# Performance work log

Measured on AMD Instinct MI355X. Metric: run time of the kernel, lower is better.

The kernel has to match this reference:

```python
import jax, jax.numpy as jnp
import numpy as np

EPS = 1e-8

def setup_inputs() -> dict:
    key = jax.random.key(0)
    k1, k2, k3 = jax.random.split(key, 3)
    b, c, h, w = 64, 20, 128, 128
    x = jax.random.normal(k1, (b, c, h, w), dtype=jnp.float32)
    y = jax.random.randint(k2, (b, c), 0, 2).astype(jnp.int32)
    threshold_p = jnp.zeros((b, c, h * w), dtype=jnp.float32)
    fg = jax.random.uniform(k3, (b, c), dtype=jnp.float32)
    return {"x": x, "y": y, "threshold_p": threshold_p, "fg": fg, "iter": 0}

def reference(x, y, threshold_p, fg, iter):
    b, c, h, w = x.shape
    hw = h * w
    xs = jax.nn.sigmoid(x.reshape(b, c, hw))  # [b,c,hw]
    yf = y.astype(xs.dtype)
    if iter % 100 < 80:
        # per-row descending sort, pick the fg*(h*w)-th value as threshold
        srt = -jnp.sort(-xs.reshape(b * c, hw), axis=1)  # descending
        idx = (fg.reshape(-1) * hw).astype(jnp.int32)  # [b*c]
        thr = jnp.take_along_axis(srt, idx[:, None], axis=1).reshape(b, c, 1)
        thr = jax.lax.stop_gradient(thr)
    else:
        thr = jax.nn.sigmoid(jnp.mean(threshold_p.reshape(b, c, hw), axis=2))[:, :, None]
        xs = jax.lax.stop_gradient(xs)
    thr = jnp.clip(thr, 0.0001)  # [b,c,1], broadcasts over hw
    y_ = yf[:, :, None]  # [b,c,1] broadcast equivalent of stacking hw copies
    mask_low = jax.lax.stop_gradient((xs <= thr).astype(xs.dtype) * y_)
    mask_high = jax.lax.stop_gradient((xs > thr).astype(xs.dtype) * y_)
    h_low = (-(xs * xs) / (thr * thr) + 2.0 * xs / thr) * mask_low
    alpha = 1.0 / jnp.clip((1.0 - thr) ** 2, EPS)
    h_high = alpha * (1.0 - xs) * (1.0 - 2.0 * thr + xs) * mask_high
    if iter % 100 < 80:
        neg_loss = -(1.0 - y_) * jnp.log(jnp.clip(1.0 - xs, EPS))
        loss = jnp.mean(h_high + h_low + neg_loss)
    else:
        loss = jnp.sum(h_low) / jnp.sum(mask_low) + jnp.sum(h_high) / jnp.sum(mask_high)
    return loss
```

## Files before the change

### kernel.cpp

```cpp
#include <hip/hip_runtime.h>

#define HW     16384
#define NROWS  1280
#define NT     512
#define NWAVES (NT / 64)
#define CAP    1024
#define NBIN1  4096

__device__ __forceinline__ unsigned f2u(float f) {
    unsigned u = __float_as_uint(f);
    unsigned m = (unsigned)((int)u >> 31);
    return u ^ (m | 0x80000000u);
}
__device__ __forceinline__ float u2f(unsigned u) {
    u = (u & 0x80000000u) ? (u & 0x7fffffffu) : ~u;
    return __uint_as_float(u);
}

__device__ __forceinline__ void wave_scan_pick(
    const unsigned* h, int bins_per_lane, int stride, unsigned kk,
    unsigned* s_bin, unsigned* s_k)
{
    const int lane = threadIdx.x & 63;
    const int base = lane * bins_per_lane;
    unsigned local = 0;
    for (int j = 0; j < bins_per_lane; ++j) {
        int b = base + j;
        local += h[stride * b] + (stride == 2 ? h[stride * b + 1] : 0u);
    }
    unsigned s = local;
    #pragma unroll
    for (int off = 1; off < 64; off <<= 1) {
        unsigned t = __shfl_down(s, off, 64);
        if (lane + off < 64) s += t;
    }
    const unsigned above = s - local;
    if (s > kk && above <= kk) {
        unsigned run = above;
        for (int j = bins_per_lane - 1; j >= 0; --j) {
            int b = base + j;
            unsigned c = h[stride * b] + (stride == 2 ? h[stride * b + 1] : 0u);
            if (run + c > kk) { *s_bin = (unsigned)b; *s_k = kk - run; break; }
            run += c;
        }
    }
}

__global__ __launch_bounds__(NT) void spatial_bce_row(
    const float* __restrict__ x, const int* __restrict__ y,
    const float* __restrict__ fg, double* __restrict__ partial)
{
    __shared__ unsigned hist[NBIN1 * 2];
    __shared__ unsigned buf[CAP];
    __shared__ unsigned s_cnt, s_bin, s_k;
    __shared__ float    swf[NWAVES][4];
    __shared__ int      swi[NWAVES];
    __shared__ double   swd[NWAVES];

    const int row  = blockIdx.x;
    const int tid  = threadIdx.x;
    const int lane = tid & 63;
    const int wid  = tid >> 6;
    const float4* x4 = (const float4*)(x + (size_t)row * HW);
    const float L2E   = 1.44269504f;
    const float LN2   = 0.69314718f;
    const float NLCAP = 18.420680744f;

    const int yrow = y[row];

    if (yrow == 0) {
        float a0 = 0.f, a1 = 0.f, a2 = 0.f, a3 = 0.f;
        for (int i = tid; i < HW / 4; i += NT) {
            float4 v = x4[i];
            a0 += fminf(v.x + LN2 * log2f(1.f + exp2f(-L2E * v.x)), NLCAP);
            a1 += fminf(v.y + LN2 * log2f(1.f + exp2f(-L2E * v.y)), NLCAP);
            a2 += fminf(v.z + LN2 * log2f(1.f + exp2f(-L2E * v.z)), NLCAP);
            a3 += fminf(v.w + LN2 * log2f(1.f + exp2f(-L2E * v.w)), NLCAP);
        }
        double acc = (double)((a0 + a1) + (a2 + a3));
        #pragma unroll
        for (int off = 32; off > 0; off >>= 1) acc += __shfl_down(acc, off, 64);
        if (lane == 0) swd[wid] = acc;
        __syncthreads();
        if (tid == 0) {
            double t = 0.0;
            for (int w = 0; w < NWAVES; ++w) t += swd[w];
            partial[row] = t;
        }
        return;
    }

    {
        uint4 z = {0u, 0u, 0u, 0u};
        for (int i = tid; i < NBIN1 * 2 / 4; i += NT) ((uint4*)hist)[i] = z;
    }
    if (tid == 0) {
        int k = (int)(fg[row] * (float)HW);
        k = max(0, min(HW - 1, k));
        s_k = (unsigned)k; s_cnt = 0u;
    }
    __syncthreads();
    const unsigned k0 = s_k;

    const int rep = tid & 1;
    for (int i = tid; i < HW / 4; i += NT) {
        float4 v = x4[i];
        atomicAdd(&hist[2 * (f2u(v.x) >> 20) + rep], 1u);
        atomicAdd(&hist[2 * (f2u(v.y) >> 20) + rep], 1u);
        atomicAdd(&hist[2 * (f2u(v.z) >> 20) + rep], 1u);
        atomicAdd(&hist[2 * (f2u(v.w) >> 20) + rep], 1u);
    }
    __syncthreads();
    if (tid < 64) wave_scan_pick(hist, NBIN1 / 64, 2, k0, &s_bin, &s_k);
    __syncthreads();
    const unsigned bin1 = s_bin;
    const unsigned k1   = s_k;

    float sL = 0.f, s2L = 0.f, sH = 0.f, s2H = 0.f;
    int   nH = 0;
    for (int i = tid; i < HW / 4; i += NT) {
        float4 v = x4[i];
        float e[4] = {v.x, v.y, v.z, v.w};
        #pragma unroll
        for (int j = 0; j < 4; ++j) {
            float xv = e[j];
            unsigned u = f2u(xv);
            unsigned b = u >> 20;
            float t  = exp2f(-L2E * xv);
            float s  = __builtin_amdgcn_rcpf(1.0f + t);
            float s2 = s * s;
            if (b < bin1)      { sL += s; s2L += s2; }
            else if (b > bin1) { sH += s; s2H += s2; ++nH; }
            else { unsigned p = atomicAdd(&s_cnt, 1u); if (p < CAP) buf[p] = u; }
        }
    }
    __syncthreads();
    const unsigned cnt = s_cnt;

    unsigned ustar;
    if (cnt <= CAP) {
        for (int i = tid; i < 1024; i += NT) hist[i] = 0u;
        __syncthreads();
        for (int c = tid; c < (int)cnt; c += NT)
            atomicAdd(&hist[(buf[c] >> 10) & 1023u], 1u);
        __syncthreads();
        if (tid < 64) wave_scan_pick(hist, 16, 1, k1, &s_bin, &s_k);
        __syncthreads();
        const unsigned pfx22 = (bin1 << 10) | s_bin;
        const unsigned k2    = s_k;
        for (int i = tid; i < 1024; i += NT) hist[i] = 0u;
        __syncthreads();
        for (int c = tid; c < (int)cnt; c += NT)
            if ((buf[c] >> 10) == pfx22) atomicAdd(&hist[buf[c] & 1023u], 1u);
        __syncthreads();
        if (tid < 64) wave_scan_pick(hist, 16, 1, k2, &s_bin, &s_k);
        __syncthreads();
        ustar = (pfx22 << 10) | s_bin;
    } else {
        for (int i = tid; i < 1024; i += NT) hist[i] = 0u;
        __syncthreads();
        for (int i = tid; i < HW / 4; i += NT) {
            float4 v = x4[i];
            unsigned u[4] = {f2u(v.x), f2u(v.y), f2u(v.z), f2u(v.w)};
            #pragma unroll
            for (int j = 0; j < 4; ++j)
                if ((u[j] >> 20) == bin1) atomicAdd(&hist[(u[j] >> 10) & 1023u], 1u);
        }
        __syncthreads();
        if (tid < 64) wave_scan_pick(hist, 16, 1, k1, &s_bin, &s_k);
        __syncthreads();
        const unsigned pfx22 = (bin1 << 10) | s_bin;
        const unsigned k2    = s_k;
        for (int i = tid; i < 1024; i += NT) hist[i] = 0u;
        __syncthreads();
        for (int i = tid; i < HW / 4; i += NT) {
            float4 v = x4[i];
            unsigned u[4] = {f2u(v.x), f2u(v.y), f2u(v.z), f2u(v.w)};
            #pragma unroll
            for (int j = 0; j < 4; ++j)
                if ((u[j] >> 10) == pfx22) atomicAdd(&hist[u[j] & 1023u], 1u);
        }
        __syncthreads();
        if (tid < 64) wave_scan_pick(hist, 16, 1, k2, &s_bin, &s_k);
        __syncthreads();
        ustar = (pfx22 << 10) | s_bin;
    }

    const float xk = u2f(ustar);
    float thr = 1.0f / (1.0f + expf(-xk));
    thr = fmaxf(thr, 1e-4f);

    if (cnt <= CAP) {
        for (int c = tid; c < (int)cnt; c += NT) {
            float xv = u2f(buf[c]);
            float t  = exp2f(-L2E * xv);
            float s  = __builtin_amdgcn_rcpf(1.0f + t);
            float s2 = s * s;
            if (s > thr) { sH += s; s2H += s2; ++nH; }
            else         { sL += s; s2L += s2; }
        }
    } else {
        for (int i = tid; i < HW / 4; i += NT) {
            float4 v = x4[i];
            float e[4] = {v.x, v.y, v.z, v.w};
            #pragma unroll
            for (int j = 0; j < 4; ++j) {
                unsigned u = f2u(e[j]);
                if ((u >> 20) == bin1) {
                    float t  = exp2f(-L2E * e[j]);
                    float s  = __builtin_amdgcn_rcpf(1.0f + t);
                    float s2 = s * s;
                    if (s > thr) { sH += s; s2H += s2; ++nH; }
                    else         { sL += s; s2L += s2; }
                }
            }
        }
    }

    #pragma unroll
    for (int off = 32; off > 0; off >>= 1) {
        sL  += __shfl_down(sL,  off, 64);
        s2L += __shfl_down(s2L, off, 64);
        sH  += __shfl_down(sH,  off, 64);
        s2H += __shfl_down(s2H, off, 64);
        nH  += __shfl_down(nH,  off, 64);
    }
    if (lane == 0) {
        swf[wid][0] = sL; swf[wid][1] = s2L; swf[wid][2] = sH; swf[wid][3] = s2H;
        swi[wid] = nH;
    }
    __syncthreads();
    if (tid == 0) {
        double SL = 0, S2L = 0, SH = 0, S2H = 0; double NH = 0;
        for (int w = 0; w < NWAVES; ++w) {
            SL += swf[w][0]; S2L += swf[w][1]; SH += swf[w][2]; S2H += swf[w][3];
            NH += (double)swi[w];
        }
        const double t   = (double)thr;
        const double omt = 1.0 - t;
        const double a   = 1.0 / fmax(omt * omt, 1e-8);
        const double low  = 2.0 * SL / t - S2L / (t * t);
        const double high = a * (NH * (1.0 - 2.0 * t) - S2H + 2.0 * t * SH);
        partial[row] = low + high;
    }
}

__global__ __launch_bounds__(256) void spatial_bce_final(
    const double* __restrict__ partial, float* __restrict__ out)
{
    __shared__ double sred[256];
    double acc = 0.0;
    for (int i = threadIdx.x; i < NROWS; i += 256) acc += partial[i];
    sred[threadIdx.x] = acc;
    __syncthreads();
    for (int off = 128; off > 0; off >>= 1) {
        if (threadIdx.x < off) sred[threadIdx.x] += sred[threadIdx.x + off];
        __syncthreads();
    }
    if (threadIdx.x == 0)
        out[0] = (float)(sred[0] / ((double)NROWS * (double)HW));
}

extern "C" void kernel_launch(void* const* d_in, const int* in_sizes, int n_in,
                              void* d_out, int out_size, void* d_ws, size_t ws_size,
                              hipStream_t stream) {
    const float* x  = (const float*)d_in[0];
    const int*   y  = (const int*)d_in[1];
    const float* fg = (const float*)d_in[3];

    double* partial = (double*)d_ws;

    spatial_bce_row<<<NROWS, NT, 0, stream>>>(x, y, fg, partial);
    spatial_bce_final<<<1, 256, 0, stream>>>(partial, (float*)d_out);
}
```

Measured before the change: 44.35 us.

## Keep row in registers and replace candidate buffer with on-the-fly sub-histograms

Each thread loads its 32 row elements into registers once and reuses them for every radix-select pass, instead of re-reading global memory each pass. The shared candidate buffer and its overflow fallback are removed. The second-level histogram is built during the moments pass and the third level from the registers, and classification compares bit keys rather than sigmoids. Shared histograms are padded to spread bank conflicts, and the softplus for negative rows is rewritten in a numerically stable form. In exchange, register pressure rises, which may lower occupancy.

```diff
diff --git a/kernel.cpp b/kernel.cpp
--- a/kernel.cpp
+++ b/kernel.cpp
@@ -4,8 +4,11 @@
 #define NROWS  1280
 #define NT     512
 #define NWAVES (NT / 64)
-#define CAP    1024
+#define NCHUNK (HW / 4 / NT)
 #define NBIN1  4096
+#define SEG1   (NBIN1 + NBIN1/32)
+#define NSUB   1024
+#define SEGS   (NSUB + NSUB/32)
 
 __device__ __forceinline__ unsigned f2u(float f) {
     unsigned u = __float_as_uint(f);
@@ -16,17 +19,20 @@
     u = (u & 0x80000000u) ? (u & 0x7fffffffu) : ~u;
     return __uint_as_float(u);
 }
+__device__ __forceinline__ int padi(int b) { return b + (b >> 5); }
 
 __device__ __forceinline__ void wave_scan_pick(
-    const unsigned* h, int bins_per_lane, int stride, unsigned kk,
+    const unsigned* h, int bpl, int rep_off, unsigned kk,
     unsigned* s_bin, unsigned* s_k)
 {
     const int lane = threadIdx.x & 63;
-    const int base = lane * bins_per_lane;
+    const int base = lane * bpl;
     unsigned local = 0;
-    for (int j = 0; j < bins_per_lane; ++j) {
-        int b = base + j;
-        local += h[stride * b] + (stride == 2 ? h[stride * b + 1] : 0u);
+    for (int j = 0; j < bpl; ++j) {
+        int a = padi(base + j);
+        unsigned c = h[a];
+        if (rep_off) c += h[rep_off + a];
+        local += c;
     }
     unsigned s = local;
     #pragma unroll
@@ -37,12 +43,49 @@
     const unsigned above = s - local;
     if (s > kk && above <= kk) {
         unsigned run = above;
-        for (int j = bins_per_lane - 1; j >= 0; --j) {
-            int b = base + j;
-            unsigned c = h[stride * b] + (stride == 2 ? h[stride * b + 1] : 0u);
-            if (run + c > kk) { *s_bin = (unsigned)b; *s_k = kk - run; break; }
+        for (int j = bpl - 1; j >= 0; --j) {
+            int a = padi(base + j);
+            unsigned c = h[a];
+            if (rep_off) c += h[rep_off + a];
+            if (run + c > kk) { *s_bin = (unsigned)(base + j); *s_k = kk - run; break; }
             run += c;
         }
+    }
+}
+
+__device__ __forceinline__ void moments_one(
+    float xv, unsigned bin1, unsigned* hsub,
+    float& sL, float& s2L, float& sH, float& s2H, int& nH)
+{
+    const float L2E = 1.44269504f;
+    unsigned u = f2u(xv);
+    unsigned b = u >> 20;
+    float t = exp2f(-L2E * xv);
+    float s = __builtin_amdgcn_rcpf(1.0f + t);
+    float s2 = s * s;
+    if (b < bin1)      { sL += s; s2L += s2; }
+    else if (b > bin1) { sH += s; s2H += s2; ++nH; }
+    else atomicAdd(&hsub[padi((u >> 10) & 1023u)], 1u);
+}
+
+__device__ __forceinline__ void micro_one(float xv, unsigned pfx22, unsigned* hsub)
+{
+    unsigned u = f2u(xv);
+    if ((u >> 10) == pfx22) atomicAdd(&hsub[padi(u & 1023u)], 1u);
+}
+
+__device__ __forceinline__ void classify_one(
+    float xv, unsigned bin1, unsigned ustar,
+    float& sL, float& s2L, float& sH, float& s2H, int& nH)
+{
+    const float L2E = 1.44269504f;
+    unsigned u = f2u(xv);
+    if ((u >> 20) == bin1) {
+        float t = exp2f(-L2E * xv);
+        float s = __builtin_amdgcn_rcpf(1.0f + t);
+        float s2 = s * s;
+        if (u > ustar) { sH += s; s2H += s2; ++nH; }
+        else           { sL += s; s2L += s2; }
     }
 }
 
@@ -50,9 +93,8 @@
     const float* __restrict__ x, const int* __restrict__ y,
     const float* __restrict__ fg, double* __restrict__ partial)
 {
-    __shared__ unsigned hist[NBIN1 * 2];
-    __shared__ unsigned buf[CAP];
-    __shared__ unsigned s_cnt, s_bin, s_k;
+    __shared__ unsigned hist[2 * SEG1];
+    __shared__ unsigned s_bin, s_k;
     __shared__ float    swf[NWAVES][4];
     __shared__ int      swi[NWAVES];
     __shared__ double   swd[NWAVES];
@@ -72,10 +114,10 @@
         float a0 = 0.f, a1 = 0.f, a2 = 0.f, a3 = 0.f;
         for (int i = tid; i < HW / 4; i += NT) {
             float4 v = x4[i];
-            a0 += fminf(v.x + LN2 * log2f(1.f + exp2f(-L2E * v.x)), NLCAP);
-            a1 += fminf(v.y + LN2 * log2f(1.f + exp2f(-L2E * v.y)), NLCAP);
-            a2 += fminf(v.z + LN2 * log2f(1.f + exp2f(-L2E * v.z)), NLCAP);
-            a3 += fminf(v.w + LN2 * log2f(1.f + exp2f(-L2E * v.w)), NLCAP);
+            a0 += fminf(fmaxf(v.x, 0.f) + LN2 * log2f(1.f + exp2f(-L2E * fabsf(v.x))), NLCAP);
+            a1 += fminf(fmaxf(v.y, 0.f) + LN2 * log2f(1.f + exp2f(-L2E * fabsf(v.y))), NLCAP);
+            a2 += fminf(fmaxf(v.z, 0.f) + LN2 * log2f(1.f + exp2f(-L2E * fabsf(v.z))), NLCAP);
+            a3 += fminf(fmaxf(v.w, 0.f) + LN2 * log2f(1.f + exp2f(-L2E * fabsf(v.w))), NLCAP);
         }
         double acc = (double)((a0 + a1) + (a2 + a3));
         #pragma unroll
@@ -90,131 +132,79 @@
         return;
     }
 
+    float4 xr[NCHUNK];
+    #pragma unroll
+    for (int it = 0; it < NCHUNK; ++it) xr[it] = x4[tid + it * NT];
+
     {
         uint4 z = {0u, 0u, 0u, 0u};
-        for (int i = tid; i < NBIN1 * 2 / 4; i += NT) ((uint4*)hist)[i] = z;
+        for (int i = tid; i < 2 * SEG1 / 4; i += NT) ((uint4*)hist)[i] = z;
     }
     if (tid == 0) {
         int k = (int)(fg[row] * (float)HW);
         k = max(0, min(HW - 1, k));
-        s_k = (unsigned)k; s_cnt = 0u;
+        s_k = (unsigned)k;
     }
     __syncthreads();
     const unsigned k0 = s_k;
 
-    const int rep = tid & 1;
-    for (int i = tid; i < HW / 4; i += NT) {
-        float4 v = x4[i];
-        atomicAdd(&hist[2 * (f2u(v.x) >> 20) + rep], 1u);
-        atomicAdd(&hist[2 * (f2u(v.y) >> 20) + rep], 1u);
-        atomicAdd(&hist[2 * (f2u(v.z) >> 20) + rep], 1u);
-        atomicAdd(&hist[2 * (f2u(v.w) >> 20) + rep], 1u);
-    }
-    __syncthreads();
-    if (tid < 64) wave_scan_pick(hist, NBIN1 / 64, 2, k0, &s_bin, &s_k);
+    unsigned* hrep = hist + (tid & 1) * SEG1;
+    #pragma unroll
+    for (int it = 0; it < NCHUNK; ++it) {
+        atomicAdd(&hrep[padi(f2u(xr[it].x) >> 20)], 1u);
+        atomicAdd(&hrep[padi(f2u(xr[it].y) >> 20)], 1u);
+        atomicAdd(&hrep[padi(f2u(xr[it].z) >> 20)], 1u);
+        atomicAdd(&hrep[padi(f2u(xr[it].w) >> 20)], 1u);
+    }
+    __syncthreads();
+    if (tid < 64) wave_scan_pick(hist, NBIN1 / 64, SEG1, k0, &s_bin, &s_k);
     __syncthreads();
     const unsigned bin1 = s_bin;
     const unsigned k1   = s_k;
 
+    for (int i = tid; i < SEGS; i += NT) hist[SEG1 + i] = 0u;
+    __syncthreads();
+
     float sL = 0.f, s2L = 0.f, sH = 0.f, s2H = 0.f;
     int   nH = 0;
-    for (int i = tid; i < HW / 4; i += NT) {
-        float4 v = x4[i];
-        float e[4] = {v.x, v.y, v.z, v.w};
-        #pragma unroll
-        for (int j = 0; j < 4; ++j) {
-            float xv = e[j];
-            unsigned u = f2u(xv);
-            unsigned b = u >> 20;
-            float t  = exp2f(-L2E * xv);
-            float s  = __builtin_amdgcn_rcpf(1.0f + t);
-            float s2 = s * s;
-            if (b < bin1)      { sL += s; s2L += s2; }
-            else if (b > bin1) { sH += s; s2H += s2; ++nH; }
-            else { unsigned p = atomicAdd(&s_cnt, 1u); if (p < CAP) buf[p] = u; }
-        }
-    }
-    __syncthreads();
-    const unsigned cnt = s_cnt;
-
-    unsigned ustar;
-    if (cnt <= CAP) {
-        for (int i = tid; i < 1024; i += NT) hist[i] = 0u;
-        __syncthreads();
-        for (int c = tid; c < (int)cnt; c += NT)
-            atomicAdd(&hist[(buf[c] >> 10) & 1023u], 1u);
-        __syncthreads();
-        if (tid < 64) wave_scan_pick(hist, 16, 1, k1, &s_bin, &s_k);
-        __syncthreads();
-        const unsigned pfx22 = (bin1 << 10) | s_bin;
-        const unsigned k2    = s_k;
-        for (int i = tid; i < 1024; i += NT) hist[i] = 0u;
-        __syncthreads();
-        for (int c = tid; c < (int)cnt; c += NT)
-            if ((buf[c] >> 10) == pfx22) atomicAdd(&hist[buf[c] & 1023u], 1u);
-        __syncthreads();
-        if (tid < 64) wave_scan_pick(hist, 16, 1, k2, &s_bin, &s_k);
-        __syncthreads();
-        ustar = (pfx22 << 10) | s_bin;
-    } else {
-        for (int i = tid; i < 1024; i += NT) hist[i] = 0u;
-        __syncthreads();
-        for (int i = tid; i < HW / 4; i += NT) {
-            float4 v = x4[i];
-            unsigned u[4] = {f2u(v.x), f2u(v.y), f2u(v.z), f2u(v.w)};
-            #pragma unroll
-            for (int j = 0; j < 4; ++j)
-                if ((u[j] >> 20) == bin1) atomicAdd(&hist[(u[j] >> 10) & 1023u], 1u);
-        }
-        __syncthreads();
-        if (tid < 64) wave_scan_pick(hist, 16, 1, k1, &s_bin, &s_k);
-        __syncthreads();
-        const unsigned pfx22 = (bin1 << 10) | s_bin;
-        const unsigned k2    = s_k;
-        for (int i = tid; i < 1024; i += NT) hist[i] = 0u;
-        __syncthreads();
-        for (int i = tid; i < HW / 4; i += NT) {
-            float4 v = x4[i];
-            unsigned u[4] = {f2u(v.x), f2u(v.y), f2u(v.z), f2u(v.w)};
-            #pragma unroll
-            for (int j = 0; j < 4; ++j)
-                if ((u[j] >> 10) == pfx22) atomicAdd(&hist[u[j] & 1023u], 1u);
-        }
-        __syncthreads();
-        if (tid < 64) wave_scan_pick(hist, 16, 1, k2, &s_bin, &s_k);
-        __syncthreads();
-        ustar = (pfx22 << 10) | s_bin;
-    }
+    unsigned* sub1 = hist + SEG1;
+    #pragma unroll
+    for (int it = 0; it < NCHUNK; ++it) {
+        moments_one(xr[it].x, bin1, sub1, sL, s2L, sH, s2H, nH);
+        moments_one(xr[it].y, bin1, sub1, sL, s2L, sH, s2H, nH);
+        moments_one(xr[it].z, bin1, sub1, sL, s2L, sH, s2H, nH);
+        moments_one(xr[it].w, bin1, sub1, sL, s2L, sH, s2H, nH);
+    }
+    __syncthreads();
+    if (tid < 64) wave_scan_pick(sub1, NSUB / 64, 0, k1, &s_bin, &s_k);
+    else for (int i = tid - 64; i < SEGS; i += NT - 64) hist[i] = 0u;
+    __syncthreads();
+    const unsigned bin2  = s_bin;
+    const unsigned k2    = s_k;
+    const unsigned pfx22 = (bin1 << 10) | bin2;
+
+    #pragma unroll
+    for (int it = 0; it < NCHUNK; ++it) {
+        micro_one(xr[it].x, pfx22, hist);
+        micro_one(xr[it].y, pfx22, hist);
+        micro_one(xr[it].z, pfx22, hist);
+        micro_one(xr[it].w, pfx22, hist);
+    }
+    __syncthreads();
+    if (tid < 64) wave_scan_pick(hist, NSUB / 64, 0, k2, &s_bin, &s_k);
+    __syncthreads();
+    const unsigned ustar = (pfx22 << 10) | s_bin;
 
     const float xk = u2f(ustar);
     float thr = 1.0f / (1.0f + expf(-xk));
     thr = fmaxf(thr, 1e-4f);
 
-    if (cnt <= CAP) {
-        for (int c = tid; c < (int)cnt; c += NT) {
-            float xv = u2f(buf[c]);
-            float t  = exp2f(-L2E * xv);
-            float s  = __builtin_amdgcn_rcpf(1.0f + t);
-            float s2 = s * s;
-            if (s > thr) { sH += s; s2H += s2; ++nH; }
-            else         { sL += s; s2L += s2; }
-        }
-    } else {
-        for (int i = tid; i < HW / 4; i += NT) {
-            float4 v = x4[i];
-            float e[4] = {v.x, v.y, v.z, v.w};
-            #pragma unroll
-            for (int j = 0; j < 4; ++j) {
-                unsigned u = f2u(e[j]);
-                if ((u >> 20) == bin1) {
-                    float t  = exp2f(-L2E * e[j]);
-                    float s  = __builtin_amdgcn_rcpf(1.0f + t);
-                    float s2 = s * s;
-                    if (s > thr) { sH += s; s2H += s2; ++nH; }
-                    else         { sL += s; s2L += s2; }
-                }
-            }
-        }
+    #pragma unroll
+    for (int it = 0; it < NCHUNK; ++it) {
+        classify_one(xr[it].x, bin1, ustar, sL, s2L, sH, s2H, nH);
+        classify_one(xr[it].y, bin1, ustar, sL, s2L, sH, s2H, nH);
+        classify_one(xr[it].z, bin1, ustar, sL, s2L, sH, s2H, nH);
+        classify_one(xr[it].w, bin1, ustar, sL, s2L, sH, s2H, nH);
     }
 
     #pragma unroll
@@ -231,7 +221,7 @@
     }
     __syncthreads();
     if (tid == 0) {
-        double SL = 0, S2L = 0, SH = 0, S2H = 0; double NH = 0;
+        double SL = 0, S2L = 0, SH = 0, S2H = 0, NH = 0;
         for (int w = 0; w < NWAVES; ++w) {
             SL += swf[w][0]; S2L += swf[w][1]; SH += swf[w][2]; S2H += swf[w][3];
             NH += (double)swi[w];
```

Result: slower. 71.65 us (+61.6%).

## Split threshold selection from moment accumulation into separate kernels

Applied to the files above, without the earlier changes.

Restructures the per-row kernel into three launches. The first does only the radix-select of the threshold for positive rows and leaves sigmoid evaluation out of its scan. The second streams each row in two half-row blocks of 256 threads and accumulates moments by comparing x against the clipped selected x value. The third combines the moments. This is meant to shorten the serial select path, balance load between y=0 and y=1 rows, and raise parallelism, at the cost of an extra launch and re-reading x. The bucket capacity also grows so the fallback full pass is taken less often.

```diff
diff --git a/kernel.cpp b/kernel.cpp
--- a/kernel.cpp
+++ b/kernel.cpp
@@ -3,8 +3,7 @@
 #define HW     16384
 #define NROWS  1280
 #define NT     512
-#define NWAVES (NT / 64)
-#define CAP    1024
+#define CAP    1536
 #define NBIN1  4096
 
 __device__ __forceinline__ unsigned f2u(float f) {
@@ -18,13 +17,13 @@
 }
 
 __device__ __forceinline__ void wave_scan_pick(
-    const unsigned* h, int bins_per_lane, int stride, unsigned kk,
+    const unsigned* h, int bpl, int stride, unsigned kk,
     unsigned* s_bin, unsigned* s_k)
 {
     const int lane = threadIdx.x & 63;
-    const int base = lane * bins_per_lane;
+    const int base = lane * bpl;
     unsigned local = 0;
-    for (int j = 0; j < bins_per_lane; ++j) {
+    for (int j = 0; j < bpl; ++j) {
         int b = base + j;
         local += h[stride * b] + (stride == 2 ? h[stride * b + 1] : 0u);
     }
@@ -37,7 +36,7 @@
     const unsigned above = s - local;
     if (s > kk && above <= kk) {
         unsigned run = above;
-        for (int j = bins_per_lane - 1; j >= 0; --j) {
+        for (int j = bpl - 1; j >= 0; --j) {
             int b = base + j;
             unsigned c = h[stride * b] + (stride == 2 ? h[stride * b + 1] : 0u);
             if (run + c > kk) { *s_bin = (unsigned)b; *s_k = kk - run; break; }
@@ -46,49 +45,20 @@
     }
 }
 
-__global__ __launch_bounds__(NT) void spatial_bce_row(
+__global__ __launch_bounds__(NT) void select_thr(
     const float* __restrict__ x, const int* __restrict__ y,
-    const float* __restrict__ fg, double* __restrict__ partial)
+    const float* __restrict__ fg, float* __restrict__ thrv,
+    float* __restrict__ xclipv)
 {
     __shared__ unsigned hist[NBIN1 * 2];
     __shared__ unsigned buf[CAP];
     __shared__ unsigned s_cnt, s_bin, s_k;
-    __shared__ float    swf[NWAVES][4];
-    __shared__ int      swi[NWAVES];
-    __shared__ double   swd[NWAVES];
-
-    const int row  = blockIdx.x;
-    const int tid  = threadIdx.x;
-    const int lane = tid & 63;
-    const int wid  = tid >> 6;
+
+    const int row = blockIdx.x;
+    if (y[row] == 0) return;
+
+    const int tid = threadIdx.x;
     const float4* x4 = (const float4*)(x + (size_t)row * HW);
-    const float L2E   = 1.44269504f;
-    const float LN2   = 0.69314718f;
-    const float NLCAP = 18.420680744f;
-
-    const int yrow = y[row];
-
-    if (yrow == 0) {
-        float a0 = 0.f, a1 = 0.f, a2 = 0.f, a3 = 0.f;
-        for (int i = tid; i < HW / 4; i += NT) {
-            float4 v = x4[i];
-            a0 += fminf(v.x + LN2 * log2f(1.f + exp2f(-L2E * v.x)), NLCAP);
-            a1 += fminf(v.y + LN2 * log2f(1.f + exp2f(-L2E * v.y)), NLCAP);
-            a2 += fminf(v.z + LN2 * log2f(1.f + exp2f(-L2E * v.z)), NLCAP);
-            a3 += fminf(v.w + LN2 * log2f(1.f + exp2f(-L2E * v.w)), NLCAP);
-        }
-        double acc = (double)((a0 + a1) + (a2 + a3));
-        #pragma unroll
-        for (int off = 32; off > 0; off >>= 1) acc += __shfl_down(acc, off, 64);
-        if (lane == 0) swd[wid] = acc;
-        __syncthreads();
-        if (tid == 0) {
-            double t = 0.0;
-            for (int w = 0; w < NWAVES; ++w) t += swd[w];
-            partial[row] = t;
-        }
-        return;
-    }
 
     {
         uint4 z = {0u, 0u, 0u, 0u};
@@ -116,23 +86,15 @@
     const unsigned bin1 = s_bin;
     const unsigned k1   = s_k;
 
-    float sL = 0.f, s2L = 0.f, sH = 0.f, s2H = 0.f;
-    int   nH = 0;
     for (int i = tid; i < HW / 4; i += NT) {
         float4 v = x4[i];
-        float e[4] = {v.x, v.y, v.z, v.w};
-        #pragma unroll
-        for (int j = 0; j < 4; ++j) {
-            float xv = e[j];
-            unsigned u = f2u(xv);
-            unsigned b = u >> 20;
-            float t  = exp2f(-L2E * xv);
-            float s  = __builtin_amdgcn_rcpf(1.0f + t);
-            float s2 = s * s;
-            if (b < bin1)      { sL += s; s2L += s2; }
-            else if (b > bin1) { sH += s; s2H += s2; ++nH; }
-            else { unsigned p = atomicAdd(&s_cnt, 1u); if (p < CAP) buf[p] = u; }
-        }
+        unsigned u[4] = {f2u(v.x), f2u(v.y), f2u(v.z), f2u(v.w)};
+        #pragma unroll
+        for (int j = 0; j < 4; ++j)
+            if ((u[j] >> 20) == bin1) {
+                unsigned p = atomicAdd(&s_cnt, 1u);
+                if (p < CAP) buf[p] = u[j];
+            }
     }
     __syncthreads();
     const unsigned cnt = s_cnt;
@@ -186,78 +148,112 @@
         ustar = (pfx22 << 10) | s_bin;
     }
 
-    const float xk = u2f(ustar);
-    float thr = 1.0f / (1.0f + expf(-xk));
-    thr = fmaxf(thr, 1e-4f);
-
-    if (cnt <= CAP) {
-        for (int c = tid; c < (int)cnt; c += NT) {
-            float xv = u2f(buf[c]);
-            float t  = exp2f(-L2E * xv);
-            float s  = __builtin_amdgcn_rcpf(1.0f + t);
-            float s2 = s * s;
-            if (s > thr) { sH += s; s2H += s2; ++nH; }
-            else         { sL += s; s2L += s2; }
+    if (tid == 0) {
+        const float xk = u2f(ustar);
+        float thr = 1.0f / (1.0f + expf(-xk));
+        thr = fmaxf(thr, 1e-4f);
+        thrv[row]   = thr;
+        xclipv[row] = fmaxf(xk, -9.2102403669f);
+    }
+}
+
+#define NT2 256
+__global__ __launch_bounds__(NT2) void moments_pass(
+    const float* __restrict__ x, const int* __restrict__ y,
+    const float* __restrict__ xclipv, double* __restrict__ mom)
+{
+    __shared__ double sw[NT2 / 64][5];
+    const int bid  = blockIdx.x;
+    const int row  = bid >> 1;
+    const int tid  = threadIdx.x;
+    const int lane = tid & 63;
+    const int wid  = tid >> 6;
+    const float4* x4 = (const float4*)(x + (size_t)row * HW + (bid & 1) * (HW / 2));
+    const float L2E   = 1.44269504f;
+    const float LN2   = 0.69314718f;
+    const float NLCAP = 18.420680744f;
+
+    float m0 = 0.f, m1 = 0.f, m2 = 0.f, m3 = 0.f, m4 = 0.f;
+    if (y[row] == 0) {
+        #pragma unroll
+        for (int i = 0; i < HW / 8 / NT2; ++i) {
+            float4 v = x4[tid + i * NT2];
+            m0 += fminf(fmaxf(v.x, 0.f) + LN2 * log2f(1.f + exp2f(-L2E * fabsf(v.x))), NLCAP);
+            m0 += fminf(fmaxf(v.y, 0.f) + LN2 * log2f(1.f + exp2f(-L2E * fabsf(v.y))), NLCAP);
+            m0 += fminf(fmaxf(v.z, 0.f) + LN2 * log2f(1.f + exp2f(-L2E * fabsf(v.z))), NLCAP);
+            m0 += fminf(fmaxf(v.w, 0.f) + LN2 * log2f(1.f + exp2f(-L2E * fabsf(v.w))), NLCAP);
         }
     } else {
-        for (int i = tid; i < HW / 4; i += NT) {
-            float4 v = x4[i];
+        const float xclip = xclipv[row];
+        #pragma unroll
+        for (int i = 0; i < HW / 8 / NT2; ++i) {
+            float4 v = x4[tid + i * NT2];
             float e[4] = {v.x, v.y, v.z, v.w};
             #pragma unroll
             for (int j = 0; j < 4; ++j) {
-                unsigned u = f2u(e[j]);
-                if ((u >> 20) == bin1) {
-                    float t  = exp2f(-L2E * e[j]);
-                    float s  = __builtin_amdgcn_rcpf(1.0f + t);
-                    float s2 = s * s;
-                    if (s > thr) { sH += s; s2H += s2; ++nH; }
-                    else         { sL += s; s2L += s2; }
-                }
+                float xv = e[j];
+                float s  = __builtin_amdgcn_rcpf(1.f + exp2f(-L2E * xv));
+                float s2 = s * s;
+                if (xv <= xclip) { m0 += s; m1 += s2; }
+                else             { m2 += s; m3 += s2; m4 += 1.f; }
             }
         }
     }
-
     #pragma unroll
     for (int off = 32; off > 0; off >>= 1) {
-        sL  += __shfl_down(sL,  off, 64);
-        s2L += __shfl_down(s2L, off, 64);
-        sH  += __shfl_down(sH,  off, 64);
-        s2H += __shfl_down(s2H, off, 64);
-        nH  += __shfl_down(nH,  off, 64);
+        m0 += __shfl_down(m0, off, 64);
+        m1 += __shfl_down(m1, off, 64);
+        m2 += __shfl_down(m2, off, 64);
+        m3 += __shfl_down(m3, off, 64);
+        m4 += __shfl_down(m4, off, 64);
     }
     if (lane == 0) {
-        swf[wid][0] = sL; swf[wid][1] = s2L; swf[wid][2] = sH; swf[wid][3] = s2H;
-        swi[wid] = nH;
+        sw[wid][0] = m0; sw[wid][1] = m1; sw[wid][2] = m2;
+        sw[wid][3] = m3; sw[wid][4] = m4;
     }
     __syncthreads();
     if (tid == 0) {
-        double SL = 0, S2L = 0, SH = 0, S2H = 0; double NH = 0;
-        for (int w = 0; w < NWAVES; ++w) {
-            SL += swf[w][0]; S2L += swf[w][1]; SH += swf[w][2]; S2H += swf[w][3];
-            NH += (double)swi[w];
-        }
-        const double t   = (double)thr;
-        const double omt = 1.0 - t;
-        const double a   = 1.0 / fmax(omt * omt, 1e-8);
-        const double low  = 2.0 * SL / t - S2L / (t * t);
-        const double high = a * (NH * (1.0 - 2.0 * t) - S2H + 2.0 * t * SH);
-        partial[row] = low + high;
-    }
-}
-
-__global__ __launch_bounds__(256) void spatial_bce_final(
-    const double* __restrict__ partial, float* __restrict__ out)
-{
-    __shared__ double sred[256];
+        double a0 = 0, a1 = 0, a2 = 0, a3 = 0, a4 = 0;
+        #pragma unroll
+        for (int w = 0; w < NT2 / 64; ++w) {
+            a0 += sw[w][0]; a1 += sw[w][1]; a2 += sw[w][2];
+            a3 += sw[w][3]; a4 += sw[w][4];
+        }
+        double* o = mom + (size_t)bid * 5;
+        o[0] = a0; o[1] = a1; o[2] = a2; o[3] = a3; o[4] = a4;
+    }
+}
+
+__global__ __launch_bounds__(NT) void combine_final(
+    const int* __restrict__ y, const float* __restrict__ thrv,
+    const double* __restrict__ mom, float* __restrict__ out)
+{
+    __shared__ double sred[NT];
+    const int tid = threadIdx.x;
     double acc = 0.0;
-    for (int i = threadIdx.x; i < NROWS; i += 256) acc += partial[i];
-    sred[threadIdx.x] = acc;
-    __syncthreads();
-    for (int off = 128; off > 0; off >>= 1) {
-        if (threadIdx.x < off) sred[threadIdx.x] += sred[threadIdx.x + off];
-        __syncthreads();
-    }
-    if (threadIdx.x == 0)
+    for (int r = tid; r < NROWS; r += NT) {
+        const double* a = mom + (size_t)(2 * r) * 5;
+        const double* b = a + 5;
+        if (y[r] == 0) {
+            acc += a[0] + b[0];
+        } else {
+            double SL = a[0] + b[0], S2L = a[1] + b[1];
+            double SH = a[2] + b[2], S2H = a[3] + b[3];
+            double NH = a[4] + b[4];
+            double t   = (double)thrv[r];
+            double omt = 1.0 - t;
+            double al  = 1.0 / fmax(omt * omt, 1e-8);
+            acc += 2.0 * SL / t - S2L / (t * t)
+                 + al * (NH * (1.0 - 2.0 * t) + 2.0 * t * SH - S2H);
+        }
+    }
+    sred[tid] = acc;
+    __syncthreads();
+    for (int off = NT / 2; off > 0; off >>= 1) {
+        if (tid < off) sred[tid] += sred[tid + off];
+        __syncthreads();
+    }
+    if (tid == 0)
         out[0] = (float)(sred[0] / ((double)NROWS * (double)HW));
 }
 
@@ -268,8 +264,11 @@
     const int*   y  = (const int*)d_in[1];
     const float* fg = (const float*)d_in[3];
 
-    double* partial = (double*)d_ws;
-
-    spatial_bce_row<<<NROWS, NT, 0, stream>>>(x, y, fg, partial);
-    spatial_bce_final<<<1, 256, 0, stream>>>(partial, (float*)d_out);
-}
+    float*  thrv   = (float*)d_ws;
+    float*  xclipv = thrv + NROWS;
+    double* mom    = (double*)(xclipv + NROWS);
+
+    select_thr  <<<NROWS,     NT,  0, stream>>>(x, y, fg, thrv, xclipv);
+    moments_pass<<<NROWS * 2, NT2, 0, stream>>>(x, y, xclipv, mom);
+    combine_final<<<1,        NT,  0, stream>>>(y, thrv, mom, (float*)d_out);
+}
```

Measured after the change: 51.18 us. 1.15x slower.

## Fuse sigmoid totals into histogram pass and only sum minority side

Applied to the files above, without the earlier changes.

The first histogram pass now also accumulates the total sum of sigmoid and sigmoid squared for the row. The second pass then computes sigmoids only for elements on the smaller side of the selected bin and gets the other side by subtraction. It also adds a fallback path for when the threshold clamp is active, rotates the histogram scan index per lane to reduce LDS bank conflicts, and switches the negative-row softplus to a numerically stable form. This moves transcendental work into a pass that was bound by LDS atomics. The cost is extra registers and more cancellation error in the float subtraction.

```diff
diff --git a/kernel.cpp b/kernel.cpp
--- a/kernel.cpp
+++ b/kernel.cpp
@@ -18,14 +18,14 @@
 }
 
 __device__ __forceinline__ void wave_scan_pick(
-    const unsigned* h, int bins_per_lane, int stride, unsigned kk,
-    unsigned* s_bin, unsigned* s_k)
+    const unsigned* h, int bpl, int stride, unsigned kk,
+    unsigned* s_bin, unsigned* s_k, unsigned* s_cbin)
 {
     const int lane = threadIdx.x & 63;
-    const int base = lane * bins_per_lane;
+    const int base = lane * bpl;
     unsigned local = 0;
-    for (int j = 0; j < bins_per_lane; ++j) {
-        int b = base + j;
+    for (int j = 0; j < bpl; ++j) {
+        int b = base + ((j + lane) & (bpl - 1));
         local += h[stride * b] + (stride == 2 ? h[stride * b + 1] : 0u);
     }
     unsigned s = local;
@@ -37,10 +37,14 @@
     const unsigned above = s - local;
     if (s > kk && above <= kk) {
         unsigned run = above;
-        for (int j = bins_per_lane - 1; j >= 0; --j) {
+        for (int j = bpl - 1; j >= 0; --j) {
             int b = base + j;
             unsigned c = h[stride * b] + (stride == 2 ? h[stride * b + 1] : 0u);
-            if (run + c > kk) { *s_bin = (unsigned)b; *s_k = kk - run; break; }
+            if (run + c > kk) {
+                *s_bin = (unsigned)b; *s_k = kk - run;
+                if (s_cbin) *s_cbin = c;
+                break;
+            }
             run += c;
         }
     }
@@ -52,9 +56,8 @@
 {
     __shared__ unsigned hist[NBIN1 * 2];
     __shared__ unsigned buf[CAP];
-    __shared__ unsigned s_cnt, s_bin, s_k;
-    __shared__ float    swf[NWAVES][4];
-    __shared__ int      swi[NWAVES];
+    __shared__ unsigned s_cnt, s_bin, s_k, s_cbin;
+    __shared__ float    swf[NWAVES][9];
     __shared__ double   swd[NWAVES];
 
     const int row  = blockIdx.x;
@@ -72,10 +75,10 @@
         float a0 = 0.f, a1 = 0.f, a2 = 0.f, a3 = 0.f;
         for (int i = tid; i < HW / 4; i += NT) {
             float4 v = x4[i];
-            a0 += fminf(v.x + LN2 * log2f(1.f + exp2f(-L2E * v.x)), NLCAP);
-            a1 += fminf(v.y + LN2 * log2f(1.f + exp2f(-L2E * v.y)), NLCAP);
-            a2 += fminf(v.z + LN2 * log2f(1.f + exp2f(-L2E * v.z)), NLCAP);
-            a3 += fminf(v.w + LN2 * log2f(1.f + exp2f(-L2E * v.w)), NLCAP);
+            a0 += fminf(fmaxf(v.x, 0.f) + LN2 * log2f(1.f + exp2f(-L2E * fabsf(v.x))), NLCAP);
+            a1 += fminf(fmaxf(v.y, 0.f) + LN2 * log2f(1.f + exp2f(-L2E * fabsf(v.y))), NLCAP);
+            a2 += fminf(fmaxf(v.z, 0.f) + LN2 * log2f(1.f + exp2f(-L2E * fabsf(v.z))), NLCAP);
+            a3 += fminf(fmaxf(v.w, 0.f) + LN2 * log2f(1.f + exp2f(-L2E * fabsf(v.w))), NLCAP);
         }
         double acc = (double)((a0 + a1) + (a2 + a3));
         #pragma unroll
@@ -102,36 +105,43 @@
     __syncthreads();
     const unsigned k0 = s_k;
 
+    float S1 = 0.f, S2 = 0.f;
     const int rep = tid & 1;
-    for (int i = tid; i < HW / 4; i += NT) {
-        float4 v = x4[i];
-        atomicAdd(&hist[2 * (f2u(v.x) >> 20) + rep], 1u);
-        atomicAdd(&hist[2 * (f2u(v.y) >> 20) + rep], 1u);
-        atomicAdd(&hist[2 * (f2u(v.z) >> 20) + rep], 1u);
-        atomicAdd(&hist[2 * (f2u(v.w) >> 20) + rep], 1u);
-    }
-    __syncthreads();
-    if (tid < 64) wave_scan_pick(hist, NBIN1 / 64, 2, k0, &s_bin, &s_k);
-    __syncthreads();
-    const unsigned bin1 = s_bin;
-    const unsigned k1   = s_k;
-
-    float sL = 0.f, s2L = 0.f, sH = 0.f, s2H = 0.f;
-    int   nH = 0;
     for (int i = tid; i < HW / 4; i += NT) {
         float4 v = x4[i];
         float e[4] = {v.x, v.y, v.z, v.w};
         #pragma unroll
         for (int j = 0; j < 4; ++j) {
-            float xv = e[j];
-            unsigned u = f2u(xv);
+            unsigned u = f2u(e[j]);
+            atomicAdd(&hist[2 * (u >> 20) + rep], 1u);
+            float s = __builtin_amdgcn_rcpf(1.f + exp2f(-L2E * e[j]));
+            S1 += s; S2 += s * s;
+        }
+    }
+    __syncthreads();
+    if (tid < 64) wave_scan_pick(hist, NBIN1 / 64, 2, k0, &s_bin, &s_k, &s_cbin);
+    __syncthreads();
+    const unsigned bin1   = s_bin;
+    const unsigned k1     = s_k;
+    const unsigned cbin   = s_cbin;
+    const unsigned nAbove = k0 - k1;
+    const bool highMinor  = (2u * nAbove + cbin <= (unsigned)HW);
+
+    float mS = 0.f, mS2 = 0.f;
+    for (int i = tid; i < HW / 4; i += NT) {
+        float4 v = x4[i];
+        float e[4] = {v.x, v.y, v.z, v.w};
+        #pragma unroll
+        for (int j = 0; j < 4; ++j) {
+            unsigned u = f2u(e[j]);
             unsigned b = u >> 20;
-            float t  = exp2f(-L2E * xv);
-            float s  = __builtin_amdgcn_rcpf(1.0f + t);
-            float s2 = s * s;
-            if (b < bin1)      { sL += s; s2L += s2; }
-            else if (b > bin1) { sH += s; s2H += s2; ++nH; }
-            else { unsigned p = atomicAdd(&s_cnt, 1u); if (p < CAP) buf[p] = u; }
+            if (b == bin1) {
+                unsigned p = atomicAdd(&s_cnt, 1u);
+                if (p < CAP) buf[p] = u;
+            } else if (highMinor ? (b > bin1) : (b < bin1)) {
+                float s = __builtin_amdgcn_rcpf(1.f + exp2f(-L2E * e[j]));
+                mS += s; mS2 += s * s;
+            }
         }
     }
     __syncthreads();
@@ -144,7 +154,7 @@
         for (int c = tid; c < (int)cnt; c += NT)
             atomicAdd(&hist[(buf[c] >> 10) & 1023u], 1u);
         __syncthreads();
-        if (tid < 64) wave_scan_pick(hist, 16, 1, k1, &s_bin, &s_k);
+        if (tid < 64) wave_scan_pick(hist, 16, 1, k1, &s_bin, &s_k, 0);
         __syncthreads();
         const unsigned pfx22 = (bin1 << 10) | s_bin;
         const unsigned k2    = s_k;
@@ -153,7 +163,7 @@
         for (int c = tid; c < (int)cnt; c += NT)
             if ((buf[c] >> 10) == pfx22) atomicAdd(&hist[buf[c] & 1023u], 1u);
         __syncthreads();
-        if (tid < 64) wave_scan_pick(hist, 16, 1, k2, &s_bin, &s_k);
+        if (tid < 64) wave_scan_pick(hist, 16, 1, k2, &s_bin, &s_k, 0);
         __syncthreads();
         ustar = (pfx22 << 10) | s_bin;
     } else {
@@ -167,7 +177,7 @@
                 if ((u[j] >> 20) == bin1) atomicAdd(&hist[(u[j] >> 10) & 1023u], 1u);
         }
         __syncthreads();
-        if (tid < 64) wave_scan_pick(hist, 16, 1, k1, &s_bin, &s_k);
+        if (tid < 64) wave_scan_pick(hist, 16, 1, k1, &s_bin, &s_k, 0);
         __syncthreads();
         const unsigned pfx22 = (bin1 << 10) | s_bin;
         const unsigned k2    = s_k;
@@ -181,7 +191,7 @@
                 if ((u[j] >> 10) == pfx22) atomicAdd(&hist[u[j] & 1023u], 1u);
         }
         __syncthreads();
-        if (tid < 64) wave_scan_pick(hist, 16, 1, k2, &s_bin, &s_k);
+        if (tid < 64) wave_scan_pick(hist, 16, 1, k2, &s_bin, &s_k, 0);
         __syncthreads();
         ustar = (pfx22 << 10) | s_bin;
     }
@@ -189,17 +199,20 @@
     const float xk = u2f(ustar);
     float thr = 1.0f / (1.0f + expf(-xk));
     thr = fmaxf(thr, 1e-4f);
-
-    if (cnt <= CAP) {
+    const unsigned uclip = max(ustar, f2u(-9.2102403669f));
+    const bool clipOff   = (uclip == ustar);
+
+    float cHs = 0.f, cHs2 = 0.f, cLs = 0.f, cLs2 = 0.f, nHc = 0.f;
+    if (clipOff && cnt <= CAP) {
         for (int c = tid; c < (int)cnt; c += NT) {
-            float xv = u2f(buf[c]);
-            float t  = exp2f(-L2E * xv);
-            float s  = __builtin_amdgcn_rcpf(1.0f + t);
+            unsigned u = buf[c];
+            float xv = u2f(u);
+            float s  = __builtin_amdgcn_rcpf(1.f + exp2f(-L2E * xv));
             float s2 = s * s;
-            if (s > thr) { sH += s; s2H += s2; ++nH; }
-            else         { sL += s; s2L += s2; }
-        }
-    } else {
+            if (u > uclip) { cHs += s; cHs2 += s2; nHc += 1.f; }
+            else           { cLs += s; cLs2 += s2; }
+        }
+    } else if (clipOff) {
         for (int i = tid; i < HW / 4; i += NT) {
             float4 v = x4[i];
             float e[4] = {v.x, v.y, v.z, v.w};
@@ -207,41 +220,70 @@
             for (int j = 0; j < 4; ++j) {
                 unsigned u = f2u(e[j]);
                 if ((u >> 20) == bin1) {
-                    float t  = exp2f(-L2E * e[j]);
-                    float s  = __builtin_amdgcn_rcpf(1.0f + t);
+                    float s  = __builtin_amdgcn_rcpf(1.f + exp2f(-L2E * e[j]));
                     float s2 = s * s;
-                    if (s > thr) { sH += s; s2H += s2; ++nH; }
-                    else         { sL += s; s2L += s2; }
+                    if (u > uclip) { cHs += s; cHs2 += s2; nHc += 1.f; }
+                    else           { cLs += s; cLs2 += s2; }
                 }
             }
         }
+    } else {
+        for (int i = tid; i < HW / 4; i += NT) {
+            float4 v = x4[i];
+            float e[4] = {v.x, v.y, v.z, v.w};
+            #pragma unroll
+            for (int j = 0; j < 4; ++j) {
+                unsigned u = f2u(e[j]);
+                if (u > uclip) {
+                    float s = __builtin_amdgcn_rcpf(1.f + exp2f(-L2E * e[j]));
+                    cHs += s; cHs2 += s * s; nHc += 1.f;
+                }
+            }
+        }
     }
 
     #pragma unroll
     for (int off = 32; off > 0; off >>= 1) {
-        sL  += __shfl_down(sL,  off, 64);
-        s2L += __shfl_down(s2L, off, 64);
-        sH  += __shfl_down(sH,  off, 64);
-        s2H += __shfl_down(s2H, off, 64);
-        nH  += __shfl_down(nH,  off, 64);
+        S1  += __shfl_down(S1,  off, 64);
+        S2  += __shfl_down(S2,  off, 64);
+        mS  += __shfl_down(mS,  off, 64);
+        mS2 += __shfl_down(mS2, off, 64);
+        cHs += __shfl_down(cHs, off, 64);
+        cHs2+= __shfl_down(cHs2,off, 64);
+        cLs += __shfl_down(cLs, off, 64);
+        cLs2+= __shfl_down(cLs2,off, 64);
+        nHc += __shfl_down(nHc, off, 64);
     }
     if (lane == 0) {
-        swf[wid][0] = sL; swf[wid][1] = s2L; swf[wid][2] = sH; swf[wid][3] = s2H;
-        swi[wid] = nH;
+        swf[wid][0] = S1;  swf[wid][1] = S2;  swf[wid][2] = mS;
+        swf[wid][3] = mS2; swf[wid][4] = cHs; swf[wid][5] = cHs2;
+        swf[wid][6] = cLs; swf[wid][7] = cLs2; swf[wid][8] = nHc;
     }
     __syncthreads();
     if (tid == 0) {
-        double SL = 0, S2L = 0, SH = 0, S2H = 0; double NH = 0;
-        for (int w = 0; w < NWAVES; ++w) {
-            SL += swf[w][0]; S2L += swf[w][1]; SH += swf[w][2]; S2H += swf[w][3];
-            NH += (double)swi[w];
-        }
+        double r[9];
+        for (int q = 0; q < 9; ++q) {
+            double a = 0.0;
+            for (int w = 0; w < NWAVES; ++w) a += (double)swf[w][q];
+            r[q] = a;
+        }
+        const double tS1 = r[0], tS2 = r[1], tmS = r[2], tmS2 = r[3];
+        const double hS  = r[4], hS2 = r[5], lS  = r[6], lS2  = r[7];
+        double SH, S2H, NH;
+        if (!clipOff) {
+            SH = hS; S2H = hS2; NH = r[8];
+        } else if (highMinor) {
+            SH = tmS + hS; S2H = tmS2 + hS2; NH = (double)nAbove + r[8];
+        } else {
+            SH = tS1 - (tmS + lS); S2H = tS2 - (tmS2 + lS2);
+            NH = (double)nAbove + r[8];
+        }
+        const double SL = tS1 - SH, S2L = tS2 - S2H;
         const double t   = (double)thr;
         const double omt = 1.0 - t;
-        const double a   = 1.0 / fmax(omt * omt, 1e-8);
-        const double low  = 2.0 * SL / t - S2L / (t * t);
-        const double high = a * (NH * (1.0 - 2.0 * t) - S2H + 2.0 * t * SH);
-        partial[row] = low + high;
+        const double al  = 1.0 / fmax(omt * omt, 1e-8);
+        partial[row] = 2.0 * SL / t - S2L / (t * t)
+                     + al * (NH * (1.0 - 2.0 * t) + 2.0 * t * SH - S2H);
     }
 }
 
```

Result: slower. 52.16 us (+17.6%).
